# Kernel optimization log

Hardware: AMD Instinct MI355X
Metric: run time of the kernel (lower is better)

The kernel has to match this reference:

```python
import jax, jax.numpy as jnp
import numpy as np

DIM = 1024
NUM_HEADS = 16
HEAD_DIM = DIM // NUM_HEADS
SCALE = HEAD_DIM ** -0.5


def setup_inputs() -> dict:
    key = jax.random.key(0)
    ks = jax.random.split(key, 6)
    B, N, C = 2, 2048, DIM
    std = C ** -0.5
    return {
        "x_t": jax.random.normal(ks[0], (B, N, C), dtype=jnp.float32),
        "x_s": jax.random.normal(ks[1], (B, N, C), dtype=jnp.float32),
        "W_q": jax.random.normal(ks[2], (C, C), dtype=jnp.float32) * std,
        "W_kv": jax.random.normal(ks[3], (C, 2 * C), dtype=jnp.float32) * std,
        "W_fuse": jax.random.normal(ks[4], (C, C), dtype=jnp.float32) * std,
        "b_fuse": jax.random.normal(ks[5], (C,), dtype=jnp.float32) * 0.01,
    }


def reference(x_t, x_s, W_q, W_kv, W_fuse, b_fuse):
    B, N, C = x_t.shape
    H, D = NUM_HEADS, HEAD_DIM
    # q projection (no bias, qkv_bias=False): [B,N,C] -> [B,H,N,D]
    q = (x_t @ W_q).reshape(B, N, H, D).transpose(0, 2, 1, 3)
    # kv projection: [B,N,2C] -> k,v each [B,H,N,D]
    kv = (x_s @ W_kv).reshape(B, N, 2, H, D).transpose(2, 0, 3, 1, 4)
    k, v = kv[0], kv[1]
    # attention scores [B,H,N,N]
    attn = jnp.einsum("bhnd,bhmd->bhnm", q, k) * SCALE
    attn = jax.nn.softmax(attn, axis=-1)
    # weighted values -> [B,N,C]
    a = jnp.einsum("bhnm,bhmd->bhnd", attn, v).transpose(0, 2, 1, 3).reshape(B, N, C)
    # fuse projection (with bias); dropouts are identity (p=0)
    return a @ W_fuse + b_fuse
```

## Files before the change

kernel.cpp:

```cpp
#include <hip/hip_runtime.h>

#define SEQ 2048

typedef short short8 __attribute__((ext_vector_type(8)));
typedef float floatx4 __attribute__((ext_vector_type(4)));
typedef unsigned short ushort4v __attribute__((ext_vector_type(4)));
typedef unsigned int uint2v __attribute__((ext_vector_type(2)));
typedef __fp16 f16x4 __attribute__((ext_vector_type(4)));

static __device__ __forceinline__ unsigned short f2bf(float f) {
    unsigned int u = __builtin_bit_cast(unsigned int, f);
    u = (u + 0x7fffu + ((u >> 16) & 1u)) >> 16;
    return (unsigned short)u;
}

#if __has_builtin(__builtin_amdgcn_cvt_pk_bf16_f32)
typedef __bf16 bf16x2 __attribute__((ext_vector_type(2)));
static __device__ __forceinline__ unsigned int pk_bf16(float a, float b) {
    bf16x2 v = __builtin_amdgcn_cvt_pk_bf16_f32(a, b);
    return __builtin_bit_cast(unsigned int, v);
}
#else
static __device__ __forceinline__ unsigned int pk_bf16(float a, float b) {
    return (unsigned int)f2bf(a) | ((unsigned int)f2bf(b) << 16);
}
#endif

static __device__ __forceinline__ unsigned int pk_f16(float a, float b) {
    auto v = __builtin_amdgcn_cvt_pkrtz(a, b);
    return __builtin_bit_cast(unsigned int, v);
}

#define GLD16(gp, lp)                                                        \
    __builtin_amdgcn_global_load_lds(                                        \
        (const __attribute__((address_space(1))) unsigned int*)(gp),         \
        (__attribute__((address_space(3))) unsigned int*)(lp), 16, 0, 0)

__global__ void cvt2_kernel(const float4* __restrict__ a, const float4* __restrict__ b,
                            ushort4* __restrict__ oa, ushort4* __restrict__ ob, float sa) {
    int i = blockIdx.x * blockDim.x + threadIdx.x;
    if (i < 1048576) {
        float4 v = a[i];
        ushort4 o;
        o.x = f2bf(v.x * sa); o.y = f2bf(v.y * sa);
        o.z = f2bf(v.z * sa); o.w = f2bf(v.w * sa);
        oa[i] = o;
    } else {
        int j = i - 1048576;
        float4 v = b[j];
        ushort4 o;
        o.x = f2bf(v.x); o.y = f2bf(v.y);
        o.z = f2bf(v.z); o.w = f2bf(v.w);
        ob[j] = o;
    }
}

__global__ void transpose_all(const float* __restrict__ Wq, const float* __restrict__ Wkv,
                              const float* __restrict__ Wf,
                              unsigned short* __restrict__ oq, unsigned short* __restrict__ okv,
                              unsigned short* __restrict__ of_) {
    __shared__ float tile[32][33];
    int bx = blockIdx.x;
    const float* in; unsigned short* out; int N, t;
    if (bx < 1024)      { in = Wq;  out = oq;  N = 1024; t = bx; }
    else if (bx < 3072) { in = Wkv; out = okv; N = 2048; t = bx - 1024; }
    else                { in = Wf;  out = of_; N = 1024; t = bx - 3072; }
    int nb = N >> 5;
    int n0 = (t % nb) * 32, k0 = (t / nb) * 32;
    int tx = threadIdx.x, ty = threadIdx.y;
#pragma unroll
    for (int i = 0; i < 4; i++)
        tile[ty + i * 8][tx] = in[(size_t)(k0 + ty + i * 8) * N + n0 + tx];
    __syncthreads();
#pragma unroll
    for (int i = 0; i < 4; i++)
        out[(size_t)(n0 + ty + i * 8) * 1024 + k0 + tx] = f2bf(tile[tx][ty + i * 8]);
}

__global__ __launch_bounds__(256, 3)
void gemm_qkv(const unsigned short* __restrict__ xt,
              const unsigned short* __restrict__ xs,
              const unsigned short* __restrict__ wq,
              const unsigned short* __restrict__ wkv,
              unsigned short* __restrict__ q_ws,
              unsigned short* __restrict__ k_ws,
              unsigned short* __restrict__ vt_ws) {
    __shared__ unsigned short sA[128][64];
    __shared__ unsigned short sB[128][64];
    int tid = threadIdx.x, wave = tid >> 6, lane = tid & 63;
    int l15 = lane & 15, quad = lane >> 4;
    int cx = blockIdx.x;
    bool isq = cx < 8;
    const unsigned short* A  = isq ? xt : xs;
    const unsigned short* Bt = isq ? wq : wkv;
    int C0 = (isq ? cx : cx - 8) * 128;
    int R0 = blockIdx.y * 128;
    int wr = (wave >> 1) * 64, wc = (wave & 1) * 64;
    int srow = lane >> 3, scol = (lane & 7) * 8;

    floatx4 acc[4][4];
#pragma unroll
    for (int i = 0; i < 4; i++)
#pragma unroll
        for (int j = 0; j < 4; j++) acc[i][j] = (floatx4){0.f, 0.f, 0.f, 0.f};

    for (int kt = 0; kt < 16; kt++) {
        __syncthreads();
#pragma unroll
        for (int c = 0; c < 4; c++) {
            int rb = wave * 32 + c * 8;
            GLD16(&A [(size_t)(R0 + rb + srow) * 1024 + kt * 64 + scol], &sA[rb][0]);
            GLD16(&Bt[(size_t)(C0 + rb + srow) * 1024 + kt * 64 + scol], &sB[rb][0]);
        }
        __syncthreads();
#pragma unroll
        for (int ks = 0; ks < 2; ks++) {
            short8 af[4], bf[4];
#pragma unroll
            for (int mt = 0; mt < 4; mt++)
                af[mt] = *(const short8*)&sA[wr + mt * 16 + l15][ks * 32 + quad * 8];
#pragma unroll
            for (int nt = 0; nt < 4; nt++)
                bf[nt] = *(const short8*)&sB[wc + nt * 16 + l15][ks * 32 + quad * 8];
#pragma unroll
            for (int mt = 0; mt < 4; mt++)
#pragma unroll
                for (int nt = 0; nt < 4; nt++)
                    acc[mt][nt] = __builtin_amdgcn_mfma_f32_16x16x32_bf16(af[mt], bf[nt], acc[mt][nt], 0, 0, 0);
        }
    }

    int b = R0 >> 11, nb0 = (R0 & 2047) + wr;
#pragma unroll
    for (int mt = 0; mt < 4; mt++) {
#pragma unroll
        for (int nt = 0; nt < 4; nt++) {
            int col = C0 + wc + nt * 16 + l15;
            if (isq) {
                int h = col >> 6, d = col & 63;
#pragma unroll
                for (int r = 0; r < 4; r++) {
                    int n = nb0 + mt * 16 + quad * 4 + r;
                    q_ws[((size_t)((b * 16 + h) * 2048 + n)) * 64 + d] = f2bf(acc[mt][nt][r]);
                }
            } else if (col < 1024) {
                int h = col >> 6, d = col & 63;
#pragma unroll
                for (int r = 0; r < 4; r++) {
                    int n = nb0 + mt * 16 + quad * 4 + r;
                    k_ws[((size_t)((b * 16 + h) * 2048 + n)) * 64 + (d ^ ((n & 7) << 3))] = f2bf(acc[mt][nt][r]);
                }
            } else {
                int cc = col - 1024, h = cc >> 6, d = cc & 63;
                int n0 = nb0 + mt * 16 + quad * 4;
                int coln = (n0 & ~63) | ((n0 & 63) ^ ((d & 7) << 3));
                uint2v pk;
                pk.x = pk_f16(acc[mt][nt][0], acc[mt][nt][1]);
                pk.y = pk_f16(acc[mt][nt][2], acc[mt][nt][3]);
                *(uint2v*)&vt_ws[((size_t)((b * 16 + h) * 64 + d)) * 2048 + coln] = pk;
            }
        }
    }
}

__global__ __launch_bounds__(256, 3)
void gemm_fuse(const unsigned short* __restrict__ A,
               const unsigned short* __restrict__ Bt,
               float* __restrict__ out, const float* __restrict__ bias) {
    __shared__ unsigned short sA[128][64];
    __shared__ unsigned short sB[64][64];
    int tid = threadIdx.x, wave = tid >> 6, lane = tid & 63;
    int l15 = lane & 15, quad = lane >> 4;
    int R0 = blockIdx.y * 128, C0 = blockIdx.x * 64;
    int wr = (wave >> 1) * 64, wc = (wave & 1) * 32;
    int srow = lane >> 3, scol = (lane & 7) * 8;

    floatx4 acc[4][2];
#pragma unroll
    for (int i = 0; i < 4; i++)
#pragma unroll
        for (int j = 0; j < 2; j++) acc[i][j] = (floatx4){0.f, 0.f, 0.f, 0.f};

    for (int kt = 0; kt < 16; kt++) {
        __syncthreads();
#pragma unroll
        for (int c = 0; c < 4; c++) {
            int rb = wave * 32 + c * 8;
            GLD16(&A[(size_t)(R0 + rb + srow) * 1024 + kt * 64 + scol], &sA[rb][0]);
        }
#pragma unroll
        for (int c = 0; c < 2; c++) {
            int rb = wave * 16 + c * 8;
            GLD16(&Bt[(size_t)(C0 + rb + srow) * 1024 + kt * 64 + scol], &sB[rb][0]);
        }
        __syncthreads();
#pragma unroll
        for (int ks = 0; ks < 2; ks++) {
            short8 af[4], bf[2];
#pragma unroll
            for (int mt = 0; mt < 4; mt++)
                af[mt] = *(const short8*)&sA[wr + mt * 16 + l15][ks * 32 + quad * 8];
#pragma unroll
            for (int nt = 0; nt < 2; nt++)
                bf[nt] = *(const short8*)&sB[wc + nt * 16 + l15][ks * 32 + quad * 8];
#pragma unroll
            for (int mt = 0; mt < 4; mt++)
#pragma unroll
                for (int nt = 0; nt < 2; nt++)
                    acc[mt][nt] = __builtin_amdgcn_mfma_f32_16x16x32_bf16(af[mt], bf[nt], acc[mt][nt], 0, 0, 0);
        }
    }

#pragma unroll
    for (int mt = 0; mt < 4; mt++) {
#pragma unroll
        for (int r = 0; r < 4; r++) {
            int row = R0 + wr + mt * 16 + quad * 4 + r;
#pragma unroll
            for (int nt = 0; nt < 2; nt++) {
                int col = C0 + wc + nt * 16 + l15;
                out[(size_t)row * 1024 + col] = acc[mt][nt][r] + bias[col];
            }
        }
    }
}

__global__ __launch_bounds__(256, 2)
void attn_kernel(const unsigned short* __restrict__ Q,
                 const unsigned short* __restrict__ K,
                 const unsigned short* __restrict__ Vt,
                 unsigned short* __restrict__ Aout) {
    __shared__ __align__(16) unsigned short smem[16384];
    __shared__ float lred[4][4][16];

    int tid = threadIdx.x, wave = tid >> 6, lane = tid & 63;
    int l15 = lane & 15, quad = lane >> 4;

    int id = blockIdx.x;
    int logical = (id & 7) * 128 + (id >> 3);
    int bh = logical >> 5, qt = logical & 31;
    int b = bh >> 4, h = bh & 15;
    int qr0 = qt * 64;

    const unsigned short* Qp = Q + (size_t)bh * SEQ * 64;
    const unsigned short* Kp = K + (size_t)bh * SEQ * 64;
    const unsigned short* Vp = Vt + (size_t)bh * 64 * SEQ;

    int srow = lane >> 3, scol = (lane & 7) * 8;
    int wk0 = wave * 16;

#define STAGE(tile, pbase)                                                    \
    {                                                                         \
        _Pragma("unroll")                                                     \
        for (int j = 0; j < 2; j++) {                                         \
            int rb = wk0 + j * 8;                                             \
            GLD16(&Kp[(size_t)((tile) * 64 + rb + srow) * 64 + scol],         \
                  &smem[(pbase) + rb * 64]);                                  \
            GLD16(&Vp[(size_t)(rb + srow) * 2048 + (tile) * 64 + scol],       \
                  &smem[8192 + (pbase) + rb * 64]);                           \
        }                                                                     \
    }

    short8 qf[4][2];
#pragma unroll
    for (int nt = 0; nt < 4; nt++)
#pragma unroll
        for (int ks = 0; ks < 2; ks++)
            qf[nt][ks] = *(const short8*)&Qp[(size_t)(qr0 + nt * 16 + l15) * 64 + ks * 32 + quad * 8];

    STAGE(0, 0)
    STAGE(1, 4096)

    floatx4 of[4][4];
#pragma unroll
    for (int i = 0; i < 4; i++)
#pragma unroll
        for (int j = 0; j < 4; j++) of[i][j] = (floatx4){0.f, 0.f, 0.f, 0.f};
    float lsum[4] = {0.f, 0.f, 0.f, 0.f};

    int krow = wk0 + l15;
    int ksw = (l15 & 7) << 3;
    int kaddr0 = krow * 64 + ((quad * 8) ^ ksw);
    int kaddr1 = krow * 64 + ((32 + quad * 8) ^ ksw);
    int vcol = (wk0 + quad * 4) ^ ksw;

    asm volatile("s_waitcnt vmcnt(0)" ::: "memory");
    __syncthreads();

    auto compute = [&](int pb) {
        __builtin_amdgcn_s_setprio(1);
        short8 kf0 = *(const short8*)&smem[pb + kaddr0];
        short8 kf1 = *(const short8*)&smem[pb + kaddr1];
        f16x4 pf[4];
#pragma unroll
        for (int nt = 0; nt < 4; nt++) {
            floatx4 zero = (floatx4){0.f, 0.f, 0.f, 0.f};
            floatx4 s = __builtin_amdgcn_mfma_f32_16x16x32_bf16(kf0, qf[nt][0], zero, 0, 0, 0);
            s = __builtin_amdgcn_mfma_f32_16x16x32_bf16(kf1, qf[nt][1], s, 0, 0, 0);
            float p0 = __builtin_amdgcn_exp2f(s[0]);
            float p1 = __builtin_amdgcn_exp2f(s[1]);
            float p2 = __builtin_amdgcn_exp2f(s[2]);
            float p3 = __builtin_amdgcn_exp2f(s[3]);
            lsum[nt] += (p0 + p1) + (p2 + p3);
            uint2v u;
            u.x = pk_f16(p0, p1);
            u.y = pk_f16(p2, p3);
            pf[nt] = __builtin_bit_cast(f16x4, u);
        }
#pragma unroll
        for (int dt = 0; dt < 4; dt++) {
            int vrow = dt * 16 + l15;
            ushort4v vv = *(const ushort4v*)&smem[8192 + pb + vrow * 64 + vcol];
            f16x4 vf = __builtin_bit_cast(f16x4, vv);
#pragma unroll
            for (int nt = 0; nt < 4; nt++)
                of[dt][nt] = __builtin_amdgcn_mfma_f32_16x16x16f16(vf, pf[nt], of[dt][nt], 0, 0, 0);
        }
        __builtin_amdgcn_s_setprio(0);
    };

#pragma unroll 2
    for (int kt = 0; kt < 30; kt++) {
        int pb = (kt & 1) * 4096;
        compute(pb);
        __builtin_amdgcn_sched_barrier(0);
        asm volatile("s_barrier" ::: "memory");
        STAGE(kt + 2, pb)
        asm volatile("s_waitcnt vmcnt(4)" ::: "memory");
        asm volatile("s_barrier" ::: "memory");
        __builtin_amdgcn_sched_barrier(0);
    }
    compute(0);
    asm volatile("s_waitcnt vmcnt(0)" ::: "memory");
    asm volatile("s_barrier" ::: "memory");
    compute(4096);
#undef STAGE

#pragma unroll
    for (int nt = 0; nt < 4; nt++) {
        float l = lsum[nt];
        l += __shfl_xor(l, 16, 64);
        l += __shfl_xor(l, 32, 64);
        lsum[nt] = l;
    }
    if (quad == 0) {
#pragma unroll
        for (int nt = 0; nt < 4; nt++) lred[wave][nt][l15] = lsum[nt];
    }
    __syncthreads();

    float* red = (float*)smem;

#define RED_WRITE(C, DTC)                                                          \
    _Pragma("unroll")                                                              \
    for (int nt = 0; nt < 4; nt++)                                                 \
        *(floatx4*)&red[((C) * 4 + wave) * 1024 + nt * 256 + lane * 4] = of[DTC][nt];

#define RED_STORE(DT, C, W0, W1, W2)                                               \
    {                                                                              \
        size_t obase = (size_t)(b * SEQ + qr0) * 1024 + h * 64 + (DT) * 16 + quad * 4; \
        _Pragma("unroll")                                                          \
        for (int nt = 0; nt < 4; nt++) {                                           \
            floatx4 a0 = *(const floatx4*)&red[((C) * 4 + (W0)) * 1024 + nt * 256 + lane * 4]; \
            floatx4 a1 = *(const floatx4*)&red[((C) * 4 + (W1)) * 1024 + nt * 256 + lane * 4]; \
            floatx4 a2 = *(const floatx4*)&red[((C) * 4 + (W2)) * 1024 + nt * 256 + lane * 4]; \
            floatx4 s = of[DT][nt] + a0 + a1 + a2;                                 \
            float lt = lred[0][nt][l15] + lred[1][nt][l15] + lred[2][nt][l15] + lred[3][nt][l15]; \
            float inv = 1.f / lt;                                                  \
            uint2v o;                                                              \
            o.x = pk_bf16(s[0] * inv, s[1] * inv);                                 \
            o.y = pk_bf16(s[2] * inv, s[3] * inv);                                 \
            *(uint2v*)&Aout[obase + (size_t)(nt * 16 + l15) * 1024] = o;           \
        }                                                                          \
    }

    RED_WRITE(0, 0)
    RED_WRITE(1, 1)
    __syncthreads();
    if (wave == 0)      RED_STORE(0, 0, 1, 2, 3)
    else if (wave == 1) RED_STORE(1, 1, 0, 2, 3)
    __syncthreads();
    RED_WRITE(0, 2)
    RED_WRITE(1, 3)
    __syncthreads();
    if (wave == 2)      RED_STORE(2, 0, 0, 1, 3)
    else if (wave == 3) RED_STORE(3, 1, 0, 1, 2)
#undef RED_WRITE
#undef RED_STORE
}

extern "C" void kernel_launch(void* const* d_in, const int* in_sizes, int n_in,
                              void* d_out, int out_size, void* d_ws, size_t ws_size,
                              hipStream_t stream) {
    const float* x_t  = (const float*)d_in[0];
    const float* x_s  = (const float*)d_in[1];
    const float* W_q  = (const float*)d_in[2];
    const float* W_kv = (const float*)d_in[3];
    const float* W_f  = (const float*)d_in[4];
    const float* b_f  = (const float*)d_in[5];
    float* out = (float*)d_out;

    char* ws = (char*)d_ws;
    const size_t MB = 1u << 20;
    unsigned short* xt_bf = (unsigned short*)(ws);
    unsigned short* xs_bf = (unsigned short*)(ws + 8 * MB);
    unsigned short* wq_t  = (unsigned short*)(ws + 16 * MB);
    unsigned short* wkv_t = (unsigned short*)(ws + 18 * MB);
    unsigned short* wf_t  = (unsigned short*)(ws + 22 * MB);
    unsigned short* q_ws  = (unsigned short*)(ws + 24 * MB);
    unsigned short* k_ws  = (unsigned short*)(ws + 32 * MB);
    unsigned short* vt_ws = (unsigned short*)(ws + 40 * MB);
    unsigned short* a_ws  = (unsigned short*)(ws + 48 * MB);

    cvt2_kernel<<<8192, 256, 0, stream>>>((const float4*)x_t, (const float4*)x_s,
                                          (ushort4*)xt_bf, (ushort4*)xs_bf,
                                          0.125f * 1.44269504088896340736f);
    transpose_all<<<4096, dim3(32, 8), 0, stream>>>(W_q, W_kv, W_f, wq_t, wkv_t, wf_t);

    gemm_qkv<<<dim3(24, 32), 256, 0, stream>>>(xt_bf, xs_bf, wq_t, wkv_t, q_ws, k_ws, vt_ws);
    attn_kernel<<<1024, 256, 0, stream>>>(q_ws, k_ws, vt_ws, a_ws);
    gemm_fuse<<<dim3(16, 32), 256, 0, stream>>>(a_ws, wf_t, out, b_f);
}
```

Baseline: 213.9 us.

## Process key tiles in pairs with 16x16x32 f16 MFMA and MFMA row sums

The attention kernel now handles two 64-key tiles per iteration. The P·V product uses the wider 16x16x32 f16 MFMA instead of the 16x16x16 one, with V fragments built from both tiles. The row sum of exp scores is computed by an MFMA against a ones vector instead of scalar adds and cross-lane shuffles. Staging becomes four buffers deep (doubled LDS, 64 KB), which issues more global loads per barrier but may cut occupancy and raise register pressure.

```diff
diff --git a/kernel.cpp b/kernel.cpp
--- a/kernel.cpp
+++ b/kernel.cpp
@@ -4,9 +4,9 @@
 
 typedef short short8 __attribute__((ext_vector_type(8)));
 typedef float floatx4 __attribute__((ext_vector_type(4)));
-typedef unsigned short ushort4v __attribute__((ext_vector_type(4)));
 typedef unsigned int uint2v __attribute__((ext_vector_type(2)));
-typedef __fp16 f16x4 __attribute__((ext_vector_type(4)));
+typedef unsigned int uint4v __attribute__((ext_vector_type(4)));
+typedef __fp16 f16x8 __attribute__((ext_vector_type(8)));
 
 static __device__ __forceinline__ unsigned short f2bf(float f) {
     unsigned int u = __builtin_bit_cast(unsigned int, f);
@@ -230,7 +230,7 @@
                  const unsigned short* __restrict__ K,
                  const unsigned short* __restrict__ Vt,
                  unsigned short* __restrict__ Aout) {
-    __shared__ __align__(16) unsigned short smem[16384];
+    __shared__ __align__(16) unsigned short smem[32768];
     __shared__ float lred[4][4][16];
 
     int tid = threadIdx.x, wave = tid >> 6, lane = tid & 63;
@@ -249,15 +249,15 @@
     int srow = lane >> 3, scol = (lane & 7) * 8;
     int wk0 = wave * 16;
 
-#define STAGE(tile, pbase)                                                    \
+#define STAGE(tile, kb)                                                       \
     {                                                                         \
         _Pragma("unroll")                                                     \
         for (int j = 0; j < 2; j++) {                                         \
             int rb = wk0 + j * 8;                                             \
             GLD16(&Kp[(size_t)((tile) * 64 + rb + srow) * 64 + scol],         \
-                  &smem[(pbase) + rb * 64]);                                  \
+                  &smem[(kb) + rb * 64]);                                     \
             GLD16(&Vp[(size_t)(rb + srow) * 2048 + (tile) * 64 + scol],       \
-                  &smem[8192 + (pbase) + rb * 64]);                           \
+                  &smem[16384 + (kb) + rb * 64]);                             \
         }                                                                     \
     }
 
@@ -268,15 +268,20 @@
         for (int ks = 0; ks < 2; ks++)
             qf[nt][ks] = *(const short8*)&Qp[(size_t)(qr0 + nt * 16 + l15) * 64 + ks * 32 + quad * 8];
 
-    STAGE(0, 0)
-    STAGE(1, 4096)
+    STAGE(0, 0) STAGE(1, 4096) STAGE(2, 8192) STAGE(3, 12288)
 
     floatx4 of[4][4];
 #pragma unroll
     for (int i = 0; i < 4; i++)
 #pragma unroll
         for (int j = 0; j < 4; j++) of[i][j] = (floatx4){0.f, 0.f, 0.f, 0.f};
-    float lsum[4] = {0.f, 0.f, 0.f, 0.f};
+    floatx4 of_l[4];
+#pragma unroll
+    for (int i = 0; i < 4; i++) of_l[i] = (floatx4){0.f, 0.f, 0.f, 0.f};
+
+    f16x8 vones;
+#pragma unroll
+    for (int i = 0; i < 8; i++) vones[i] = (__fp16)1.0f;
 
     int krow = wk0 + l15;
     int ksw = (l15 & 7) << 3;
@@ -287,65 +292,74 @@
     asm volatile("s_waitcnt vmcnt(0)" ::: "memory");
     __syncthreads();
 
-    auto compute = [&](int pb) {
+    auto compute_pair = [&](int kb) {
         __builtin_amdgcn_s_setprio(1);
-        short8 kf0 = *(const short8*)&smem[pb + kaddr0];
-        short8 kf1 = *(const short8*)&smem[pb + kaddr1];
-        f16x4 pf[4];
+        uint2v pka[4], pkb[4];
+        {
+            short8 kf0 = *(const short8*)&smem[kb + kaddr0];
+            short8 kf1 = *(const short8*)&smem[kb + kaddr1];
+#pragma unroll
+            for (int nt = 0; nt < 4; nt++) {
+                floatx4 z = (floatx4){0.f, 0.f, 0.f, 0.f};
+                floatx4 s = __builtin_amdgcn_mfma_f32_16x16x32_bf16(kf0, qf[nt][0], z, 0, 0, 0);
+                s = __builtin_amdgcn_mfma_f32_16x16x32_bf16(kf1, qf[nt][1], s, 0, 0, 0);
+                pka[nt].x = pk_f16(__builtin_amdgcn_exp2f(s[0]), __builtin_amdgcn_exp2f(s[1]));
+                pka[nt].y = pk_f16(__builtin_amdgcn_exp2f(s[2]), __builtin_amdgcn_exp2f(s[3]));
+            }
+        }
+        {
+            short8 kf0 = *(const short8*)&smem[kb + 4096 + kaddr0];
+            short8 kf1 = *(const short8*)&smem[kb + 4096 + kaddr1];
+#pragma unroll
+            for (int nt = 0; nt < 4; nt++) {
+                floatx4 z = (floatx4){0.f, 0.f, 0.f, 0.f};
+                floatx4 s = __builtin_amdgcn_mfma_f32_16x16x32_bf16(kf0, qf[nt][0], z, 0, 0, 0);
+                s = __builtin_amdgcn_mfma_f32_16x16x32_bf16(kf1, qf[nt][1], s, 0, 0, 0);
+                pkb[nt].x = pk_f16(__builtin_amdgcn_exp2f(s[0]), __builtin_amdgcn_exp2f(s[1]));
+                pkb[nt].y = pk_f16(__builtin_amdgcn_exp2f(s[2]), __builtin_amdgcn_exp2f(s[3]));
+            }
+        }
+#pragma unroll
+        for (int dt = 0; dt < 4; dt++) {
+            int vbase = 16384 + kb + (dt * 16 + l15) * 64 + vcol;
+            uint2v va = *(const uint2v*)&smem[vbase];
+            uint2v vb = *(const uint2v*)&smem[vbase + 4096];
+            f16x8 vf = __builtin_bit_cast(f16x8, (uint4v){va.x, va.y, vb.x, vb.y});
+#pragma unroll
+            for (int nt = 0; nt < 4; nt++) {
+                f16x8 pf = __builtin_bit_cast(f16x8, (uint4v){pka[nt].x, pka[nt].y, pkb[nt].x, pkb[nt].y});
+                of[dt][nt] = __builtin_amdgcn_mfma_f32_16x16x32_f16(vf, pf, of[dt][nt], 0, 0, 0);
+            }
+        }
 #pragma unroll
         for (int nt = 0; nt < 4; nt++) {
-            floatx4 zero = (floatx4){0.f, 0.f, 0.f, 0.f};
-            floatx4 s = __builtin_amdgcn_mfma_f32_16x16x32_bf16(kf0, qf[nt][0], zero, 0, 0, 0);
-            s = __builtin_amdgcn_mfma_f32_16x16x32_bf16(kf1, qf[nt][1], s, 0, 0, 0);
-            float p0 = __builtin_amdgcn_exp2f(s[0]);
-            float p1 = __builtin_amdgcn_exp2f(s[1]);
-            float p2 = __builtin_amdgcn_exp2f(s[2]);
-            float p3 = __builtin_amdgcn_exp2f(s[3]);
-            lsum[nt] += (p0 + p1) + (p2 + p3);
-            uint2v u;
-            u.x = pk_f16(p0, p1);
-            u.y = pk_f16(p2, p3);
-            pf[nt] = __builtin_bit_cast(f16x4, u);
-        }
-#pragma unroll
-        for (int dt = 0; dt < 4; dt++) {
-            int vrow = dt * 16 + l15;
-            ushort4v vv = *(const ushort4v*)&smem[8192 + pb + vrow * 64 + vcol];
-            f16x4 vf = __builtin_bit_cast(f16x4, vv);
-#pragma unroll
-            for (int nt = 0; nt < 4; nt++)
-                of[dt][nt] = __builtin_amdgcn_mfma_f32_16x16x16f16(vf, pf[nt], of[dt][nt], 0, 0, 0);
+            f16x8 pf = __builtin_bit_cast(f16x8, (uint4v){pka[nt].x, pka[nt].y, pkb[nt].x, pkb[nt].y});
+            of_l[nt] = __builtin_amdgcn_mfma_f32_16x16x32_f16(vones, pf, of_l[nt], 0, 0, 0);
         }
         __builtin_amdgcn_s_setprio(0);
     };
 
 #pragma unroll 2
-    for (int kt = 0; kt < 30; kt++) {
-        int pb = (kt & 1) * 4096;
-        compute(pb);
+    for (int p = 0; p < 14; p++) {
+        int kb = (p & 1) * 8192;
+        compute_pair(kb);
         __builtin_amdgcn_sched_barrier(0);
         asm volatile("s_barrier" ::: "memory");
-        STAGE(kt + 2, pb)
-        asm volatile("s_waitcnt vmcnt(4)" ::: "memory");
+        STAGE(2 * p + 4, kb)
+        STAGE(2 * p + 5, kb + 4096)
+        asm volatile("s_waitcnt vmcnt(8)" ::: "memory");
         asm volatile("s_barrier" ::: "memory");
         __builtin_amdgcn_sched_barrier(0);
     }
-    compute(0);
+    compute_pair(0);
     asm volatile("s_waitcnt vmcnt(0)" ::: "memory");
     asm volatile("s_barrier" ::: "memory");
-    compute(4096);
+    compute_pair(8192);
 #undef STAGE
 
-#pragma unroll
-    for (int nt = 0; nt < 4; nt++) {
-        float l = lsum[nt];
-        l += __shfl_xor(l, 16, 64);
-        l += __shfl_xor(l, 32, 64);
-        lsum[nt] = l;
-    }
     if (quad == 0) {
 #pragma unroll
-        for (int nt = 0; nt < 4; nt++) lred[wave][nt][l15] = lsum[nt];
+        for (int nt = 0; nt < 4; nt++) lred[wave][nt][l15] = of_l[nt][0];
     }
     __syncthreads();
 
```

Result: faster. 201.4 us (-5.9%).
